# Kernel optimization log

Hardware: AMD Instinct MI355X
Metric: run time of the kernel (lower is better)

The kernel has to match this reference:

```python
import jax, jax.numpy as jnp
import numpy as np

T, B, D_IN, E, HA, HB, D_OUT = 64, 64, 4096, 128, 128, 128, 4096


def setup_inputs() -> dict:
    key = jax.random.key(0)
    ks = jax.random.split(key, 18)

    def u(k, shape, fan):
        b = 1.0 / np.sqrt(fan)
        return jax.random.uniform(k, shape, jnp.float32, -b, b)

    return {
        "x": jax.random.uniform(ks[0], (T, B, D_IN), jnp.float32),
        "W_emb": u(ks[1], (E, D_IN), D_IN), "b_emb": u(ks[2], (E,), D_IN),
        "W_ih_a": u(ks[3], (3 * HA, E), HA), "W_hh_a": u(ks[4], (3 * HA, HA), HA),
        "b_ih_a": u(ks[5], (3 * HA,), HA), "b_hh_a": u(ks[6], (3 * HA,), HA),
        "W_ih_b": u(ks[7], (3 * HB, E), HB), "W_hh_b": u(ks[8], (3 * HB, HB), HB),
        "b_ih_b": u(ks[9], (3 * HB,), HB), "b_hh_b": u(ks[10], (3 * HB,), HB),
        "w_alpha": u(ks[11], (1, HA), HA), "b_alpha": u(ks[12], (1,), HA),
        "W_beta": u(ks[13], (E, HB), HB), "b_beta": u(ks[14], (E,), HB),
        "W_out": u(ks[15], (D_OUT, E), E), "b_out": u(ks[16], (D_OUT,), E),
    }


def _gru_states(emb, W_ih, W_hh, b_ih, b_hh):
    # For every query position i, run a GRU over the reversed prefix
    # emb[i], emb[i-1], ..., emb[0] from h0 = 0. All T queries are batched.
    # Returns hs[s, i, b, h] = hidden of query i after step s (input emb[i-s]).
    Tlen, Bsz, _ = emb.shape
    H = W_hh.shape[1]
    i_arr = jnp.arange(Tlen)

    def step(h, s):
        idx = jnp.clip(i_arr - s, 0, Tlen - 1)          # (T,) input index per query
        xs = emb[idx]                                    # (T, B, E)
        gi = xs @ W_ih.T + b_ih                          # (T, B, 3H)
        gh = h @ W_hh.T + b_hh
        i_r, i_z, i_n = jnp.split(gi, 3, axis=-1)
        h_r, h_z, h_n = jnp.split(gh, 3, axis=-1)
        r = jax.nn.sigmoid(i_r + h_r)
        z = jax.nn.sigmoid(i_z + h_z)
        n = jnp.tanh(i_n + r * h_n)
        h_new = (1.0 - z) * n + z * h
        return h_new, h_new

    h0 = jnp.zeros((Tlen, Bsz, H), emb.dtype)
    _, hs = jax.lax.scan(step, h0, jnp.arange(Tlen))
    return hs  # (S, T, B, H)


def _retain_forward(x, W_emb, b_emb, W_ih_a, W_hh_a, b_ih_a, b_hh_a,
                    W_ih_b, W_hh_b, b_ih_b, b_hh_b, w_alpha, b_alpha,
                    W_beta, b_beta, W_out, b_out):
    Tlen = x.shape[0]
    emb = x @ W_emb.T + b_emb                            # (T, B, E)

    hs_a = _gru_states(emb, W_ih_a, W_hh_a, b_ih_a, b_hh_a)  # (S, T, B, HA)
    hs_b = _gru_states(emb, W_ih_b, W_hh_b, b_ih_b, b_hh_b)  # (S, T, B, HB)

    i_arr = jnp.arange(Tlen)
    # reverse_h[i, j] = hidden after processing emb[i..j] (reverse order) = hs[i - j, i]
    rev = jnp.clip(i_arr[:, None] - i_arr[None, :], 0, Tlen - 1)  # (T, T)
    rh_a = hs_a[rev, i_arr[:, None]] * 0.5               # (T, T, B, HA)
    rh_b = hs_b[rev, i_arr[:, None]] * 0.5               # (T, T, B, HB)

    mask = (i_arr[None, :] <= i_arr[:, None])            # (T, T): j <= i valid
    logits = jnp.einsum('ijbh,h->ijb', rh_a, w_alpha[0]) + b_alpha[0]
    logits = jnp.where(mask[:, :, None], logits, -1e9)
    alpha = jax.nn.softmax(logits, axis=1)               # softmax over prefix steps j
    alpha = alpha * mask[:, :, None].astype(alpha.dtype)

    beta = jnp.tanh(rh_b @ W_beta.T + b_beta)            # (T, T, B, E)

    # c[i] = mean_{j<=i} alpha[i,j] * beta[i,j] * emb[j]
    c = jnp.einsum('ijb,ijbe->ibe', alpha, beta * emb[None, :, :, :])
    counts = jnp.arange(1, Tlen + 1, dtype=c.dtype)[:, None, None]
    c = c / counts

    return jax.nn.sigmoid(c @ W_out.T + b_out)           # (T, B, D_OUT)


def reference(x, W_emb, b_emb, W_ih_a, W_hh_a, b_ih_a, b_hh_a,
              W_ih_b, W_hh_b, b_ih_b, b_hh_b, w_alpha, b_alpha,
              W_beta, b_beta, W_out, b_out):
    return _retain_forward(x, W_emb, b_emb, W_ih_a, W_hh_a, b_ih_a, b_hh_a,
                           W_ih_b, W_hh_b, b_ih_b, b_hh_b, w_alpha, b_alpha,
                           W_beta, b_beta, W_out, b_out)
```

## Files before the change

kernel.cpp:

```cpp
#include <hip/hip_runtime.h>
#include <hip/hip_bf16.h>


typedef __attribute__((ext_vector_type(8))) short short8;
typedef __attribute__((ext_vector_type(4))) float f32x4;
typedef _Float16 half8 __attribute__((ext_vector_type(8)));

#define MFMA16(a, b, c) __builtin_amdgcn_mfma_f32_16x16x32_bf16((a), (b), (c), 0, 0, 0)

#define LOG2E 1.4426950408889634f
#define TLOG2E 2.8853900817779268f

__device__ __forceinline__ unsigned pkbf(float a, float b) {
  __hip_bfloat162 t = __float22bfloat162_rn(float2{a, b});
  return *reinterpret_cast<unsigned*>(&t);
}
__device__ __forceinline__ float ex2(float x) { return __builtin_amdgcn_exp2f(x); }
__device__ __forceinline__ float rcpa(float x) { return __builtin_amdgcn_rcpf(x); }
__device__ __forceinline__ float tanh2(float y) {
  float e = ex2(-fmaxf(y, -126.0f));
  return (1.0f - e) * rcpa(1.0f + e);
}

#define OFF_PART   0u
#define OFF_GI3    16777216u
#define OFF_EMBBF  25165824u
#define OFF_CBF    26214400u
#define OFF_WEMB   27262976u
#define OFF_WOUT   28311552u
#define OFF_WHHA   29360128u
#define OFF_WHHB   29458432u
#define OFF_WIH    29556736u
#define OFF_WBETA  29753344u

__global__ void k_prep(const float* W_emb, const float* W_out,
                       const float* W_hh_a, const float* W_hh_b,
                       const float* W_ih_a, const float* W_ih_b,
                       const float* W_beta,
                       unsigned* wemb, unsigned* wout,
                       unsigned* whha, unsigned* whhb,
                       unsigned* wih, unsigned* wbeta) {
  const unsigned total = 630784u;
  for (unsigned idx = blockIdx.x * 256u + threadIdx.x; idx < total;
       idx += gridDim.x * 256u) {
    unsigned i = idx;
    if (i < 262144u) { float2 v = ((const float2*)W_emb)[i]; wemb[i] = pkbf(v.x, v.y); continue; }
    i -= 262144u;
    if (i < 262144u) { float2 v = ((const float2*)W_out)[i]; wout[i] = pkbf(v.x, v.y); continue; }
    i -= 262144u;
    if (i < 24576u) {
      float2 v = ((const float2*)W_hh_a)[i];
      const float sc = ((i >> 13) == 2u) ? TLOG2E : LOG2E;
      whha[i] = pkbf(sc * v.x, sc * v.y); continue;
    }
    i -= 24576u;
    if (i < 24576u) {
      float2 v = ((const float2*)W_hh_b)[i];
      const float sc = ((i >> 13) == 2u) ? TLOG2E : LOG2E;
      whhb[i] = pkbf(sc * v.x, sc * v.y); continue;
    }
    i -= 24576u;
    if (i < 24576u) {
      float2 v = ((const float2*)W_ih_a)[i];
      const float sc = ((i >> 13) == 2u) ? TLOG2E : LOG2E;
      wih[i] = pkbf(sc * v.x, sc * v.y); continue;
    }
    i -= 24576u;
    if (i < 24576u) {
      float2 v = ((const float2*)W_ih_b)[i];
      const float sc = ((i >> 13) == 2u) ? TLOG2E : LOG2E;
      wih[24576u + i] = pkbf(sc * v.x, sc * v.y); continue;
    }
    i -= 24576u;
    { float2 v = ((const float2*)W_beta)[i]; wbeta[i] = pkbf(LOG2E * v.x, LOG2E * v.y); }
  }
}

__global__ __launch_bounds__(256) void k_emb_gemm(const float* __restrict__ x,
                                                  const unsigned short* __restrict__ wemb,
                                                  float* __restrict__ part) {
  const int mt = blockIdx.x >> 3, kc = blockIdx.x & 7;
  const int w = threadIdx.x >> 6, lane = threadIdx.x & 63, q = lane >> 4, ln = lane & 15;
  const f32x4 zero = {0.f, 0.f, 0.f, 0.f};
  f32x4 acc[8];
#pragma unroll
  for (int b = 0; b < 8; ++b) acc[b] = zero;

  const float* xA = x + (size_t)(mt * 64 + w * 16 + ln) * 4096 + kc * 512 + q * 8;

  for (int kk = 0; kk < 16; ++kk) {
    const int ko = kk * 32;
    float4 u0 = *(const float4*)(xA + ko);
    float4 u1 = *(const float4*)(xA + ko + 4);
    union { short8 v; unsigned u[4]; } a0;
    a0.u[0] = pkbf(u0.x, u0.y); a0.u[1] = pkbf(u0.z, u0.w);
    a0.u[2] = pkbf(u1.x, u1.y); a0.u[3] = pkbf(u1.z, u1.w);
#pragma unroll
    for (int nt = 0; nt < 8; ++nt) {
      short8 b = *(const short8*)(wemb + (size_t)(nt * 16 + ln) * 4096 + kc * 512 + ko + q * 8);
      acc[nt] = MFMA16(a0.v, b, acc[nt]);
    }
  }
  const int mbase = mt * 64 + w * 16 + q * 4;
#pragma unroll
  for (int nt = 0; nt < 8; ++nt)
#pragma unroll
    for (int r = 0; r < 4; ++r)
      part[(size_t)kc * 524288 + (size_t)(mbase + r) * 128 + nt * 16 + ln] = acc[nt][r];
}

__global__ void k_emb_reduce(const float* __restrict__ part, const float* __restrict__ b_emb,
                             _Float16* __restrict__ gih, unsigned* __restrict__ embbf) {
  const unsigned pidx = blockIdx.x * 256u + threadIdx.x;
  const unsigned e0 = (pidx * 2u) & 127u;
  const unsigned m = pidx >> 6;
  float2 s = ((const float2*)b_emb)[e0 >> 1];
#pragma unroll
  for (int kc = 0; kc < 8; ++kc) {
    float2 v = ((const float2*)(part + (size_t)kc * 524288u))[pidx];
    s.x += v.x; s.y += v.y;
  }
  gih[(size_t)m * 1024u + e0 * 8u + 6u] = (_Float16)s.x;
  gih[(size_t)m * 1024u + (e0 + 1u) * 8u + 6u] = (_Float16)s.y;
  embbf[pidx] = pkbf(s.x, s.y);
}

__global__ __launch_bounds__(256) void k_gi_gemm(const unsigned short* __restrict__ embbf,
                                                 const unsigned short* __restrict__ wih,
                                                 const float* __restrict__ b_ih_a,
                                                 const float* __restrict__ b_ih_b,
                                                 const float* __restrict__ b_hh_a,
                                                 const float* __restrict__ b_hh_b,
                                                 _Float16* __restrict__ gih) {
  const int mt = blockIdx.x / 6, nt6 = blockIdx.x % 6, nbase = nt6 * 128;
  const int w = threadIdx.x >> 6, lane = threadIdx.x & 63, q = lane >> 4, ln = lane & 15;
  const f32x4 zero = {0.f, 0.f, 0.f, 0.f};
  f32x4 acc[2][8];
#pragma unroll
  for (int a = 0; a < 2; ++a)
#pragma unroll
    for (int b = 0; b < 8; ++b) acc[a][b] = zero;

#pragma unroll
  for (int kk = 0; kk < 4; ++kk) {
    const int ko = kk * 32 + q * 8;
    short8 a0 = *(const short8*)(embbf + (size_t)(mt * 128 + (2 * w) * 16 + ln) * 128 + ko);
    short8 a1 = *(const short8*)(embbf + (size_t)(mt * 128 + (2 * w + 1) * 16 + ln) * 128 + ko);
#pragma unroll
    for (int nt = 0; nt < 8; ++nt) {
      short8 b = *(const short8*)(wih + (size_t)(nbase + nt * 16 + ln) * 128 + ko);
      acc[0][nt] = MFMA16(a0, b, acc[0][nt]);
      acc[1][nt] = MFMA16(a1, b, acc[1][nt]);
    }
  }
#pragma unroll
  for (int nt = 0; nt < 8; ++nt) {
    const int g = nbase + nt * 16 + ln;
    const int gg = g >> 7, kout = g & 127;
    float bias;
    if (g < 384) bias = b_ih_a[g] + ((gg < 2) ? b_hh_a[g] : 0.0f);
    else {
      const int g2 = g - 384;
      bias = b_ih_b[g2] + ((gg < 5) ? b_hh_b[g2] : 0.0f);
    }
    bias *= (gg == 2 || gg == 5) ? TLOG2E : LOG2E;
#pragma unroll
    for (int st = 0; st < 2; ++st) {
      const int mbase = mt * 128 + (2 * w + st) * 16 + q * 4;
#pragma unroll
      for (int r = 0; r < 4; ++r)
        gih[(size_t)(mbase + r) * 1024 + kout * 8 + gg] = (_Float16)(acc[st][nt][r] + bias);
    }
  }
}

__global__ __launch_bounds__(512) __attribute__((amdgpu_waves_per_eu(2, 2)))
void k_recur(const _Float16* __restrict__ gih,
             const unsigned short* __restrict__ whha, const unsigned short* __restrict__ whhb,
             const unsigned short* __restrict__ wbeta,
             const float* __restrict__ b_hh_a, const float* __restrict__ b_hh_b,
             const float* __restrict__ b_beta, const float* __restrict__ b_alpha,
             const float* __restrict__ w_alpha,
             const unsigned short* __restrict__ wout,
             const float* __restrict__ b_out,
             float* __restrict__ out) {
  const int tid = threadIdx.x, w = tid >> 6, lane = tid & 63, q = lane >> 4, ln = lane & 15;
  const int p = blockIdx.x >> 3, btile = blockIdx.x & 7;
  const int i1 = p, i2 = 63 - p;
  const int kout = w * 16 + ln;

  __shared__ unsigned short hA[2][16 * 136], hB[2][16 * 136];

  for (int idx = tid; idx < 16 * 136; idx += 512) { hA[0][idx] = 0; hB[0][idx] = 0; }

  const int iq = (q < 2) ? i1 : i2;
  const _Float16* gp[4];
#pragma unroll
  for (int r = 0; r < 4; ++r) {
    const int b = btile * 8 + (q & 1) * 4 + r;
    gp[r] = gih + (size_t)(iq * 64 + b) * 1024 + kout * 8;
  }

  short8 fra[3][4], frb[3][4];
#pragma unroll
  for (int g = 0; g < 3; ++g) {
    const unsigned short* ba = whha + (size_t)(g * 128 + kout) * 128;
    const unsigned short* bb = whhb + (size_t)(g * 128 + kout) * 128;
#pragma unroll
    for (int kc = 0; kc < 4; ++kc) {
      fra[g][kc] = *(const short8*)(ba + kc * 32 + q * 8);
      frb[g][kc] = *(const short8*)(bb + kc * 32 + q * 8);
    }
  }
#pragma unroll
  for (int g = 0; g < 3; ++g)
#pragma unroll
    for (int kc = 0; kc < 4; ++kc) {
      asm volatile("" : "+a"(fra[g][kc]));
      asm volatile("" : "+a"(frb[g][kc]));
    }

  short8 fbe[4];
#pragma unroll
  for (int kc = 0; kc < 4; ++kc) {
    fbe[kc] = *(const short8*)(wbeta + (size_t)(w * 16 + ln) * 128 + kc * 32 + q * 8);
    asm volatile("" : "+a"(fbe[kc]));
  }

  short8 fal[4];
#pragma unroll
  for (int kc = 0; kc < 4; ++kc) {
    float4 w0 = *(const float4*)(w_alpha + kc * 32 + q * 8);
    float4 w1 = *(const float4*)(w_alpha + kc * 32 + q * 8 + 4);
    union { short8 v; unsigned u[4]; } t;
    t.u[0] = pkbf(0.5f * LOG2E * w0.x, 0.5f * LOG2E * w0.y);
    t.u[1] = pkbf(0.5f * LOG2E * w0.z, 0.5f * LOG2E * w0.w);
    t.u[2] = pkbf(0.5f * LOG2E * w1.x, 0.5f * LOG2E * w1.y);
    t.u[3] = pkbf(0.5f * LOG2E * w1.z, 0.5f * LOG2E * w1.w);
    fal[kc] = t.v;
    asm volatile("" : "+a"(fal[kc]));
  }

  const float bhnA = TLOG2E * b_hh_a[256 + kout];
  const float bhnB = TLOG2E * b_hh_b[256 + kout];
  const float bbet = TLOG2E * b_beta[kout];
  const float bal = LOG2E * b_alpha[0];

  float hRA[4], hRB[4], cac[4], lreg[4], embp[4];
#pragma unroll
  for (int r = 0; r < 4; ++r) { hRA[r] = 0.f; hRB[r] = 0.f; cac[r] = 0.f; lreg[r] = 0.f; embp[r] = 0.f; }

  const f32x4 zero = {0.f, 0.f, 0.f, 0.f};
  int jj = iq;
  half8 ngv[4];
#pragma unroll
  for (int r = 0; r < 4; ++r) ngv[r] = *(const half8*)gp[r];

  __syncthreads();

  for (int s = 0; s <= i2; ++s) {
    const int rb = s & 1, wb = rb ^ 1;

    half8 gv[4];
#pragma unroll
    for (int r = 0; r < 4; ++r) gv[r] = ngv[r];

    short8 haf[4], hbf[4];
#pragma unroll
    for (int kc = 0; kc < 4; ++kc) {
      haf[kc] = *(const short8*)(hA[rb] + ln * 136 + kc * 32 + q * 8);
      hbf[kc] = *(const short8*)(hB[rb] + ln * 136 + kc * 32 + q * 8);
    }

    f32x4 accA[3] = {zero, zero, zero}, accB[3] = {zero, zero, zero};
    f32x4 accV = zero, accL = zero;
#pragma unroll
    for (int kc = 0; kc < 4; ++kc) {
#pragma unroll
      for (int g = 0; g < 3; ++g) {
        accA[g] = MFMA16(haf[kc], fra[g][kc], accA[g]);
        accB[g] = MFMA16(hbf[kc], frb[g][kc], accB[g]);
      }
      accV = MFMA16(hbf[kc], fbe[kc], accV);
      accL = MFMA16(haf[kc], fal[kc], accL);
    }

    const bool act = ((unsigned)(s - 1) <= (unsigned)iq);
#pragma unroll
    for (int r = 0; r < 4; ++r) {
      const float logit = accL[r] + bal;
      const float pp = act ? ex2(logit) : 0.0f;
      lreg[r] += pp;
      const float beta = tanh2(accV[r] + bbet);
      cac[r] += pp * beta * embp[r];
    }

#pragma unroll
    for (int r = 0; r < 4; ++r) {
      const int rowoff = (q * 4 + r) * 136 + kout;

      const float erA = ex2(-((float)gv[r][0] + accA[0][r]));
      const float rA = rcpa(1.0f + erA);
      const float tA = (float)gv[r][2] + rA * (accA[2][r] + bhnA);
      const float enA = ex2(-fmaxf(tA, -62.0f));
      const float ezA = ex2(-fmaxf((float)gv[r][1] + accA[1][r], -62.0f));
      const float apnA = 1.0f + enA, apzA = 1.0f + ezA;
      const float numA = fmaf(hRA[r], apnA, ezA * (1.0f - enA));
      const float hnA = numA * rcpa(apnA * apzA);
      hRA[r] = hnA;
      hA[wb][rowoff] = (unsigned short)pkbf(hnA, hnA);

      const float erB = ex2(-((float)gv[r][3] + accB[0][r]));
      const float rB = rcpa(1.0f + erB);
      const float tB = (float)gv[r][5] + rB * (accB[2][r] + bhnB);
      const float enB = ex2(-fmaxf(tB, -62.0f));
      const float ezB = ex2(-fmaxf((float)gv[r][4] + accB[1][r], -62.0f));
      const float apnB = 1.0f + enB, apzB = 1.0f + ezB;
      const float numB = fmaf(hRB[r], apnB, ezB * (1.0f - enB));
      const float hnB = numB * rcpa(apnB * apzB);
      hRB[r] = hnB;
      hB[wb][rowoff] = (unsigned short)pkbf(hnB, hnB);

      embp[r] = (float)gv[r][6];
    }

    if (jj > 0) {
      --jj;
#pragma unroll
      for (int r = 0; r < 4; ++r) gp[r] -= 65536;
    }
#pragma unroll
    for (int r = 0; r < 4; ++r) ngv[r] = *(const half8*)gp[r];

    asm volatile("s_waitcnt lgkmcnt(0)\n\ts_barrier" ::: "memory");
  }

  {
    const int rb2 = (i2 + 1) & 1;
    short8 haf[4], hbf[4];
#pragma unroll
    for (int kc = 0; kc < 4; ++kc) {
      haf[kc] = *(const short8*)(hA[rb2] + ln * 136 + kc * 32 + q * 8);
      hbf[kc] = *(const short8*)(hB[rb2] + ln * 136 + kc * 32 + q * 8);
    }
    f32x4 accV = zero, accL = zero;
#pragma unroll
    for (int kc = 0; kc < 4; ++kc) {
      accV = MFMA16(hbf[kc], fbe[kc], accV);
      accL = MFMA16(haf[kc], fal[kc], accL);
    }
    const bool act = (iq == i2);
#pragma unroll
    for (int r = 0; r < 4; ++r) {
      const float logit = accL[r] + bal;
      const float pp = act ? ex2(logit) : 0.0f;
      lreg[r] += pp;
      const float beta = tanh2(accV[r] + bbet);
      cac[r] += pp * beta * embp[r];
    }
  }

  __syncthreads();
  {
    const int crow0 = (q >= 2 ? 8 : 0) + (q & 1) * 4;
#pragma unroll
    for (int r = 0; r < 4; ++r) {
      const float val = cac[r] * rcpa(lreg[r] * (float)(iq + 1));
      hA[0][(crow0 + r) * 136 + kout] = (unsigned short)pkbf(val, val);
    }
  }
  __syncthreads();

  {
    short8 cb[4];
#pragma unroll
    for (int kc = 0; kc < 4; ++kc)
      cb[kc] = *(const short8*)(hA[0] + ln * 136 + kc * 32 + q * 8);

    const int m_glob = ((ln >= 8) ? i2 : i1) * 64 + btile * 8 + (ln & 7);
    float* orow = out + (size_t)m_glob * 4096;
    const int nb0 = w * 512;

    for (int nt = 0; nt < 32; ++nt) {
      const int n16 = nb0 + nt * 16;
      f32x4 acc = zero;
#pragma unroll
      for (int kc = 0; kc < 4; ++kc) {
        short8 a = *(const short8*)(wout + (size_t)(n16 + ln) * 128 + kc * 32 + q * 8);
        acc = MFMA16(a, cb[kc], acc);
      }
      const int n0 = n16 + q * 4;
      const float4 bo = *(const float4*)(b_out + n0);
      float4 o;
      o.x = rcpa(1.0f + ex2(-LOG2E * (acc[0] + bo.x)));
      o.y = rcpa(1.0f + ex2(-LOG2E * (acc[1] + bo.y)));
      o.z = rcpa(1.0f + ex2(-LOG2E * (acc[2] + bo.z)));
      o.w = rcpa(1.0f + ex2(-LOG2E * (acc[3] + bo.w)));
      *(float4*)(orow + n0) = o;
    }
  }
}

extern "C" void kernel_launch(void* const* d_in, const int* in_sizes, int n_in,
                              void* d_out, int out_size, void* d_ws, size_t ws_size,
                              hipStream_t stream) {
  const float* x      = (const float*)d_in[0];
  const float* W_emb  = (const float*)d_in[1];
  const float* b_emb  = (const float*)d_in[2];
  const float* W_ih_a = (const float*)d_in[3];
  const float* W_hh_a = (const float*)d_in[4];
  const float* b_ih_a = (const float*)d_in[5];
  const float* b_hh_a = (const float*)d_in[6];
  const float* W_ih_b = (const float*)d_in[7];
  const float* W_hh_b = (const float*)d_in[8];
  const float* b_ih_b = (const float*)d_in[9];
  const float* b_hh_b = (const float*)d_in[10];
  const float* w_alpha = (const float*)d_in[11];
  const float* b_alpha = (const float*)d_in[12];
  const float* W_beta = (const float*)d_in[13];
  const float* b_beta = (const float*)d_in[14];
  const float* W_out  = (const float*)d_in[15];
  const float* b_out  = (const float*)d_in[16];
  float* out = (float*)d_out;

  char* ws = (char*)d_ws;
  float*          part   = (float*)(ws + OFF_PART);
  _Float16*       gih    = (_Float16*)(ws + OFF_GI3);
  unsigned*       embbf  = (unsigned*)(ws + OFF_EMBBF);
  unsigned*       wemb   = (unsigned*)(ws + OFF_WEMB);
  unsigned*       wout   = (unsigned*)(ws + OFF_WOUT);
  unsigned*       whha   = (unsigned*)(ws + OFF_WHHA);
  unsigned*       whhb   = (unsigned*)(ws + OFF_WHHB);
  unsigned*       wih    = (unsigned*)(ws + OFF_WIH);
  unsigned*       wbeta  = (unsigned*)(ws + OFF_WBETA);

  k_prep<<<1024, 256, 0, stream>>>(W_emb, W_out, W_hh_a, W_hh_b, W_ih_a, W_ih_b,
                                   W_beta, wemb, wout, whha, whhb, wih, wbeta);
  k_emb_gemm<<<512, 256, 0, stream>>>(x, (const unsigned short*)wemb, part);
  k_emb_reduce<<<1024, 256, 0, stream>>>(part, b_emb, gih, embbf);
  k_gi_gemm<<<192, 256, 0, stream>>>((const unsigned short*)embbf, (const unsigned short*)wih,
                                     b_ih_a, b_ih_b, b_hh_a, b_hh_b, gih);
  k_recur<<<256, 512, 0, stream>>>(gih, (const unsigned short*)whha,
                                   (const unsigned short*)whhb, (const unsigned short*)wbeta,
                                   b_hh_a, b_hh_b, b_beta, b_alpha, w_alpha,
                                   (const unsigned short*)wout, b_out, out);
}
```

Measured before the change: 340.4 us.

## Re-tile embedding and input-gate GEMMs into smaller blocks; nontemporal output stores

The embedding GEMM now gives each block 16 rows instead of 64, with each wave computing two of the eight column tiles, so the grid grows from 512 to 2048 blocks. The input-gate GEMM drops from 128 to 32 rows per block and splits its column tiles across waves, growing from 192 to 768 blocks. The goal is more parallelism across CUs and fewer accumulator registers per wave. The cost is that each x row is now loaded by four waves rather than one, which adds redundant global traffic. The final output GEMM loop also gets partial unrolling and nontemporal stores to avoid polluting cache with the large output.

```diff
diff --git a/kernel.cpp b/kernel.cpp
--- a/kernel.cpp
+++ b/kernel.cpp
@@ -82,12 +82,14 @@
   const int mt = blockIdx.x >> 3, kc = blockIdx.x & 7;
   const int w = threadIdx.x >> 6, lane = threadIdx.x & 63, q = lane >> 4, ln = lane & 15;
   const f32x4 zero = {0.f, 0.f, 0.f, 0.f};
-  f32x4 acc[8];
-#pragma unroll
-  for (int b = 0; b < 8; ++b) acc[b] = zero;
-
-  const float* xA = x + (size_t)(mt * 64 + w * 16 + ln) * 4096 + kc * 512 + q * 8;
-
+  f32x4 acc[2] = {zero, zero};
+
+  const float* xA = x + (size_t)(mt * 16 + ln) * 4096 + kc * 512 + q * 8;
+  const int nt0 = w * 2;
+  const unsigned short* wb0 = wemb + (size_t)(nt0 * 16 + ln) * 4096 + kc * 512 + q * 8;
+  const unsigned short* wb1 = wb0 + (size_t)16 * 4096;
+
+#pragma unroll 4
   for (int kk = 0; kk < 16; ++kk) {
     const int ko = kk * 32;
     float4 u0 = *(const float4*)(xA + ko);
@@ -95,18 +97,17 @@
     union { short8 v; unsigned u[4]; } a0;
     a0.u[0] = pkbf(u0.x, u0.y); a0.u[1] = pkbf(u0.z, u0.w);
     a0.u[2] = pkbf(u1.x, u1.y); a0.u[3] = pkbf(u1.z, u1.w);
-#pragma unroll
-    for (int nt = 0; nt < 8; ++nt) {
-      short8 b = *(const short8*)(wemb + (size_t)(nt * 16 + ln) * 4096 + kc * 512 + ko + q * 8);
-      acc[nt] = MFMA16(a0.v, b, acc[nt]);
-    }
-  }
-  const int mbase = mt * 64 + w * 16 + q * 4;
-#pragma unroll
-  for (int nt = 0; nt < 8; ++nt)
+    short8 b0 = *(const short8*)(wb0 + ko);
+    short8 b1 = *(const short8*)(wb1 + ko);
+    acc[0] = MFMA16(a0.v, b0, acc[0]);
+    acc[1] = MFMA16(a0.v, b1, acc[1]);
+  }
+  const int mbase = mt * 16 + q * 4;
+#pragma unroll
+  for (int nt = 0; nt < 2; ++nt)
 #pragma unroll
     for (int r = 0; r < 4; ++r)
-      part[(size_t)kc * 524288 + (size_t)(mbase + r) * 128 + nt * 16 + ln] = acc[nt][r];
+      part[(size_t)kc * 524288 + (size_t)(mbase + r) * 128 + (nt0 + nt) * 16 + ln] = acc[nt][r];
 }
 
 __global__ void k_emb_reduce(const float* __restrict__ part, const float* __restrict__ b_emb,
@@ -134,28 +135,23 @@
                                                  _Float16* __restrict__ gih) {
   const int mt = blockIdx.x / 6, nt6 = blockIdx.x % 6, nbase = nt6 * 128;
   const int w = threadIdx.x >> 6, lane = threadIdx.x & 63, q = lane >> 4, ln = lane & 15;
+  const int rowg = w & 1, nth = w >> 1;
   const f32x4 zero = {0.f, 0.f, 0.f, 0.f};
-  f32x4 acc[2][8];
-#pragma unroll
-  for (int a = 0; a < 2; ++a)
-#pragma unroll
-    for (int b = 0; b < 8; ++b) acc[a][b] = zero;
+  f32x4 acc[4] = {zero, zero, zero, zero};
 
 #pragma unroll
   for (int kk = 0; kk < 4; ++kk) {
     const int ko = kk * 32 + q * 8;
-    short8 a0 = *(const short8*)(embbf + (size_t)(mt * 128 + (2 * w) * 16 + ln) * 128 + ko);
-    short8 a1 = *(const short8*)(embbf + (size_t)(mt * 128 + (2 * w + 1) * 16 + ln) * 128 + ko);
-#pragma unroll
-    for (int nt = 0; nt < 8; ++nt) {
-      short8 b = *(const short8*)(wih + (size_t)(nbase + nt * 16 + ln) * 128 + ko);
-      acc[0][nt] = MFMA16(a0, b, acc[0][nt]);
-      acc[1][nt] = MFMA16(a1, b, acc[1][nt]);
-    }
-  }
-#pragma unroll
-  for (int nt = 0; nt < 8; ++nt) {
-    const int g = nbase + nt * 16 + ln;
+    short8 a = *(const short8*)(embbf + (size_t)(mt * 32 + rowg * 16 + ln) * 128 + ko);
+#pragma unroll
+    for (int nt4 = 0; nt4 < 4; ++nt4) {
+      short8 b = *(const short8*)(wih + (size_t)(nbase + (nth * 4 + nt4) * 16 + ln) * 128 + ko);
+      acc[nt4] = MFMA16(a, b, acc[nt4]);
+    }
+  }
+#pragma unroll
+  for (int nt4 = 0; nt4 < 4; ++nt4) {
+    const int g = nbase + (nth * 4 + nt4) * 16 + ln;
     const int gg = g >> 7, kout = g & 127;
     float bias;
     if (g < 384) bias = b_ih_a[g] + ((gg < 2) ? b_hh_a[g] : 0.0f);
@@ -164,13 +160,10 @@
       bias = b_ih_b[g2] + ((gg < 5) ? b_hh_b[g2] : 0.0f);
     }
     bias *= (gg == 2 || gg == 5) ? TLOG2E : LOG2E;
-#pragma unroll
-    for (int st = 0; st < 2; ++st) {
-      const int mbase = mt * 128 + (2 * w + st) * 16 + q * 4;
-#pragma unroll
-      for (int r = 0; r < 4; ++r)
-        gih[(size_t)(mbase + r) * 1024 + kout * 8 + gg] = (_Float16)(acc[st][nt][r] + bias);
-    }
+    const int mbase = mt * 32 + rowg * 16 + q * 4;
+#pragma unroll
+    for (int r = 0; r < 4; ++r)
+      gih[(size_t)(mbase + r) * 1024 + kout * 8 + gg] = (_Float16)(acc[nt4][r] + bias);
   }
 }
 
@@ -381,6 +374,7 @@
     float* orow = out + (size_t)m_glob * 4096;
     const int nb0 = w * 512;
 
+#pragma unroll 2
     for (int nt = 0; nt < 32; ++nt) {
       const int n16 = nb0 + nt * 16;
       f32x4 acc = zero;
@@ -391,12 +385,12 @@
       }
       const int n0 = n16 + q * 4;
       const float4 bo = *(const float4*)(b_out + n0);
-      float4 o;
-      o.x = rcpa(1.0f + ex2(-LOG2E * (acc[0] + bo.x)));
-      o.y = rcpa(1.0f + ex2(-LOG2E * (acc[1] + bo.y)));
-      o.z = rcpa(1.0f + ex2(-LOG2E * (acc[2] + bo.z)));
-      o.w = rcpa(1.0f + ex2(-LOG2E * (acc[3] + bo.w)));
-      *(float4*)(orow + n0) = o;
+      f32x4 o;
+      o[0] = rcpa(1.0f + ex2(-LOG2E * (acc[0] + bo.x)));
+      o[1] = rcpa(1.0f + ex2(-LOG2E * (acc[1] + bo.y)));
+      o[2] = rcpa(1.0f + ex2(-LOG2E * (acc[2] + bo.z)));
+      o[3] = rcpa(1.0f + ex2(-LOG2E * (acc[3] + bo.w)));
+      __builtin_nontemporal_store(o, (f32x4*)(orow + n0));
     }
   }
 }
@@ -436,9 +430,9 @@
 
   k_prep<<<1024, 256, 0, stream>>>(W_emb, W_out, W_hh_a, W_hh_b, W_ih_a, W_ih_b,
                                    W_beta, wemb, wout, whha, whhb, wih, wbeta);
-  k_emb_gemm<<<512, 256, 0, stream>>>(x, (const unsigned short*)wemb, part);
+  k_emb_gemm<<<2048, 256, 0, stream>>>(x, (const unsigned short*)wemb, part);
   k_emb_reduce<<<1024, 256, 0, stream>>>(part, b_emb, gih, embbf);
-  k_gi_gemm<<<192, 256, 0, stream>>>((const unsigned short*)embbf, (const unsigned short*)wih,
+  k_gi_gemm<<<768, 256, 0, stream>>>((const unsigned short*)embbf, (const unsigned short*)wih,
                                      b_ih_a, b_ih_b, b_hh_a, b_hh_b, gih);
   k_recur<<<256, 512, 0, stream>>>(gih, (const unsigned short*)whha,
                                    (const unsigned short*)whhb, (const unsigned short*)wbeta,
```

Measured after the change: 354.5 us. +4.1%, slower.

## Fuse embedding GEMM, split-K reduction and input-gate GEMM into one front kernel

Applied to the files above, without the earlier changes.

Replaces three kernels (split-K embedding GEMM, global reduction, gate-input GEMM) with a single kernel. Each block handles 16 rows, splits K across 8 waves, reduces the partial sums in shared memory, and then runs the gate GEMM from the bf16 embedding kept in LDS. This removes the 16MB partial buffer round trip through global memory and two kernel launches. In exchange there are fewer blocks (256) with smaller M tiles, so each block re-reads W_emb more often.

```diff
diff --git a/kernel.cpp b/kernel.cpp
--- a/kernel.cpp
+++ b/kernel.cpp
@@ -22,10 +22,7 @@
   return (1.0f - e) * rcpa(1.0f + e);
 }
 
-#define OFF_PART   0u
 #define OFF_GI3    16777216u
-#define OFF_EMBBF  25165824u
-#define OFF_CBF    26214400u
 #define OFF_WEMB   27262976u
 #define OFF_WOUT   28311552u
 #define OFF_WHHA   29360128u
@@ -76,100 +73,103 @@
   }
 }
 
-__global__ __launch_bounds__(256) void k_emb_gemm(const float* __restrict__ x,
-                                                  const unsigned short* __restrict__ wemb,
-                                                  float* __restrict__ part) {
-  const int mt = blockIdx.x >> 3, kc = blockIdx.x & 7;
-  const int w = threadIdx.x >> 6, lane = threadIdx.x & 63, q = lane >> 4, ln = lane & 15;
+__global__ __launch_bounds__(512) void k_front(const float* __restrict__ x,
+                                               const unsigned short* __restrict__ wemb,
+                                               const unsigned short* __restrict__ wih,
+                                               const float* __restrict__ b_emb,
+                                               const float* __restrict__ b_ih_a,
+                                               const float* __restrict__ b_ih_b,
+                                               const float* __restrict__ b_hh_a,
+                                               const float* __restrict__ b_hh_b,
+                                               _Float16* __restrict__ gih) {
+  const int tid = threadIdx.x, w = tid >> 6, lane = tid & 63, q = lane >> 4, ln = lane & 15;
+  const int m0 = blockIdx.x * 16;
+
+  __shared__ float part[8][16][132];
+  __shared__ unsigned short embs[16][136];
+
   const f32x4 zero = {0.f, 0.f, 0.f, 0.f};
-  f32x4 acc[8];
-#pragma unroll
-  for (int b = 0; b < 8; ++b) acc[b] = zero;
-
-  const float* xA = x + (size_t)(mt * 64 + w * 16 + ln) * 4096 + kc * 512 + q * 8;
-
-  for (int kk = 0; kk < 16; ++kk) {
-    const int ko = kk * 32;
-    float4 u0 = *(const float4*)(xA + ko);
-    float4 u1 = *(const float4*)(xA + ko + 4);
-    union { short8 v; unsigned u[4]; } a0;
-    a0.u[0] = pkbf(u0.x, u0.y); a0.u[1] = pkbf(u0.z, u0.w);
-    a0.u[2] = pkbf(u1.x, u1.y); a0.u[3] = pkbf(u1.z, u1.w);
-#pragma unroll
-    for (int nt = 0; nt < 8; ++nt) {
-      short8 b = *(const short8*)(wemb + (size_t)(nt * 16 + ln) * 4096 + kc * 512 + ko + q * 8);
-      acc[nt] = MFMA16(a0.v, b, acc[nt]);
-    }
-  }
-  const int mbase = mt * 64 + w * 16 + q * 4;
-#pragma unroll
-  for (int nt = 0; nt < 8; ++nt)
-#pragma unroll
-    for (int r = 0; r < 4; ++r)
-      part[(size_t)kc * 524288 + (size_t)(mbase + r) * 128 + nt * 16 + ln] = acc[nt][r];
-}
-
-__global__ void k_emb_reduce(const float* __restrict__ part, const float* __restrict__ b_emb,
-                             _Float16* __restrict__ gih, unsigned* __restrict__ embbf) {
-  const unsigned pidx = blockIdx.x * 256u + threadIdx.x;
-  const unsigned e0 = (pidx * 2u) & 127u;
-  const unsigned m = pidx >> 6;
-  float2 s = ((const float2*)b_emb)[e0 >> 1];
-#pragma unroll
-  for (int kc = 0; kc < 8; ++kc) {
-    float2 v = ((const float2*)(part + (size_t)kc * 524288u))[pidx];
-    s.x += v.x; s.y += v.y;
-  }
-  gih[(size_t)m * 1024u + e0 * 8u + 6u] = (_Float16)s.x;
-  gih[(size_t)m * 1024u + (e0 + 1u) * 8u + 6u] = (_Float16)s.y;
-  embbf[pidx] = pkbf(s.x, s.y);
-}
-
-__global__ __launch_bounds__(256) void k_gi_gemm(const unsigned short* __restrict__ embbf,
-                                                 const unsigned short* __restrict__ wih,
-                                                 const float* __restrict__ b_ih_a,
-                                                 const float* __restrict__ b_ih_b,
-                                                 const float* __restrict__ b_hh_a,
-                                                 const float* __restrict__ b_hh_b,
-                                                 _Float16* __restrict__ gih) {
-  const int mt = blockIdx.x / 6, nt6 = blockIdx.x % 6, nbase = nt6 * 128;
-  const int w = threadIdx.x >> 6, lane = threadIdx.x & 63, q = lane >> 4, ln = lane & 15;
-  const f32x4 zero = {0.f, 0.f, 0.f, 0.f};
-  f32x4 acc[2][8];
-#pragma unroll
-  for (int a = 0; a < 2; ++a)
-#pragma unroll
-    for (int b = 0; b < 8; ++b) acc[a][b] = zero;
-
-#pragma unroll
-  for (int kk = 0; kk < 4; ++kk) {
-    const int ko = kk * 32 + q * 8;
-    short8 a0 = *(const short8*)(embbf + (size_t)(mt * 128 + (2 * w) * 16 + ln) * 128 + ko);
-    short8 a1 = *(const short8*)(embbf + (size_t)(mt * 128 + (2 * w + 1) * 16 + ln) * 128 + ko);
-#pragma unroll
-    for (int nt = 0; nt < 8; ++nt) {
-      short8 b = *(const short8*)(wih + (size_t)(nbase + nt * 16 + ln) * 128 + ko);
-      acc[0][nt] = MFMA16(a0, b, acc[0][nt]);
-      acc[1][nt] = MFMA16(a1, b, acc[1][nt]);
-    }
-  }
-#pragma unroll
-  for (int nt = 0; nt < 8; ++nt) {
-    const int g = nbase + nt * 16 + ln;
-    const int gg = g >> 7, kout = g & 127;
-    float bias;
-    if (g < 384) bias = b_ih_a[g] + ((gg < 2) ? b_hh_a[g] : 0.0f);
-    else {
-      const int g2 = g - 384;
-      bias = b_ih_b[g2] + ((gg < 5) ? b_hh_b[g2] : 0.0f);
-    }
-    bias *= (gg == 2 || gg == 5) ? TLOG2E : LOG2E;
-#pragma unroll
-    for (int st = 0; st < 2; ++st) {
-      const int mbase = mt * 128 + (2 * w + st) * 16 + q * 4;
+
+  {
+    f32x4 acc[8];
+#pragma unroll
+    for (int nt = 0; nt < 8; ++nt) acc[nt] = zero;
+
+    const float* xp = x + (size_t)(m0 + ln) * 4096 + w * 512 + q * 8;
+    const unsigned short* wp = wemb + (size_t)ln * 4096 + w * 512 + q * 8;
+
+#pragma unroll 4
+    for (int kk = 0; kk < 16; ++kk) {
+      const int ko = kk * 32;
+      float4 u0 = *(const float4*)(xp + ko);
+      float4 u1 = *(const float4*)(xp + ko + 4);
+      union { short8 v; unsigned u[4]; } a0;
+      a0.u[0] = pkbf(u0.x, u0.y); a0.u[1] = pkbf(u0.z, u0.w);
+      a0.u[2] = pkbf(u1.x, u1.y); a0.u[3] = pkbf(u1.z, u1.w);
+#pragma unroll
+      for (int nt = 0; nt < 8; ++nt) {
+        short8 b = *(const short8*)(wp + (size_t)(nt * 16) * 4096 + ko);
+        acc[nt] = MFMA16(a0.v, b, acc[nt]);
+      }
+    }
+#pragma unroll
+    for (int nt = 0; nt < 8; ++nt)
 #pragma unroll
       for (int r = 0; r < 4; ++r)
-        gih[(size_t)(mbase + r) * 1024 + kout * 8 + gg] = (_Float16)(acc[st][nt][r] + bias);
+        part[w][q * 4 + r][nt * 16 + ln] = acc[nt][r];
+  }
+  __syncthreads();
+
+  {
+    const int row = tid & 15, col0 = (tid >> 4) * 4;
+    f32x4 s = *(const f32x4*)(b_emb + col0);
+#pragma unroll
+    for (int ww = 0; ww < 8; ++ww) {
+      const f32x4 v = *(const f32x4*)&part[ww][row][col0];
+      s[0] += v[0]; s[1] += v[1]; s[2] += v[2]; s[3] += v[3];
+    }
+    _Float16* g6 = gih + (size_t)(m0 + row) * 1024 + 6;
+#pragma unroll
+    for (int j = 0; j < 4; ++j) g6[(size_t)(col0 + j) * 8] = (_Float16)s[j];
+    *(unsigned*)&embs[row][col0]     = pkbf(s[0], s[1]);
+    *(unsigned*)&embs[row][col0 + 2] = pkbf(s[2], s[3]);
+  }
+  __syncthreads();
+
+  {
+    short8 af[4];
+#pragma unroll
+    for (int kc = 0; kc < 4; ++kc)
+      af[kc] = *(const short8*)&embs[ln][kc * 32 + q * 8];
+
+    const int nb = w * 96;
+    f32x4 acg[6];
+#pragma unroll
+    for (int nt = 0; nt < 6; ++nt) acg[nt] = zero;
+
+#pragma unroll
+    for (int kc = 0; kc < 4; ++kc) {
+      const int ko = kc * 32 + q * 8;
+#pragma unroll
+      for (int nt = 0; nt < 6; ++nt) {
+        short8 b = *(const short8*)(wih + (size_t)(nb + nt * 16 + ln) * 128 + ko);
+        acg[nt] = MFMA16(af[kc], b, acg[nt]);
+      }
+    }
+#pragma unroll
+    for (int nt = 0; nt < 6; ++nt) {
+      const int g = nb + nt * 16 + ln;
+      const int gg = g >> 7, kout = g & 127;
+      float bias;
+      if (g < 384) bias = b_ih_a[g] + ((gg < 2) ? b_hh_a[g] : 0.0f);
+      else {
+        const int g2 = g - 384;
+        bias = b_ih_b[g2] + ((gg < 5) ? b_hh_b[g2] : 0.0f);
+      }
+      bias *= (gg == 2 || gg == 5) ? TLOG2E : LOG2E;
+#pragma unroll
+      for (int r = 0; r < 4; ++r)
+        gih[(size_t)(m0 + q * 4 + r) * 1024 + kout * 8 + gg] = (_Float16)(acg[nt][r] + bias);
     }
   }
 }
@@ -424,9 +424,7 @@
   float* out = (float*)d_out;
 
   char* ws = (char*)d_ws;
-  float*          part   = (float*)(ws + OFF_PART);
   _Float16*       gih    = (_Float16*)(ws + OFF_GI3);
-  unsigned*       embbf  = (unsigned*)(ws + OFF_EMBBF);
   unsigned*       wemb   = (unsigned*)(ws + OFF_WEMB);
   unsigned*       wout   = (unsigned*)(ws + OFF_WOUT);
   unsigned*       whha   = (unsigned*)(ws + OFF_WHHA);
@@ -436,10 +434,9 @@
 
   k_prep<<<1024, 256, 0, stream>>>(W_emb, W_out, W_hh_a, W_hh_b, W_ih_a, W_ih_b,
                                    W_beta, wemb, wout, whha, whhb, wih, wbeta);
-  k_emb_gemm<<<512, 256, 0, stream>>>(x, (const unsigned short*)wemb, part);
-  k_emb_reduce<<<1024, 256, 0, stream>>>(part, b_emb, gih, embbf);
-  k_gi_gemm<<<192, 256, 0, stream>>>((const unsigned short*)embbf, (const unsigned short*)wih,
-                                     b_ih_a, b_ih_b, b_hh_a, b_hh_b, gih);
+  k_front<<<256, 512, 0, stream>>>(x, (const unsigned short*)wemb,
+                                   (const unsigned short*)wih, b_emb,
+                                   b_ih_a, b_ih_b, b_hh_a, b_hh_b, gih);
   k_recur<<<256, 512, 0, stream>>>(gih, (const unsigned short*)whha,
                                    (const unsigned short*)whhb, (const unsigned short*)wbeta,
                                    b_hh_a, b_hh_b, b_beta, b_alpha, w_alpha,
```

Measured after the change: 326.6 us. 1.04x faster.
